# Performance work log

Hardware: AMD Instinct MI355X
Metric: run time of the kernel (lower is better)

## Reference

```python
import jax, jax.numpy as jnp
import numpy as np

D_MODEL = 2048
N_HEAD = 16
SEM_DIM = 1024
GEO_DIM = 1024
ATTN_DIM = 2048
ROPE_BASE = 10000.0


def _rope(x, base=ROPE_BASE):
    # x: [B, H, S, d] with even d; GPT-NeoX rotate-half convention
    S, d = x.shape[-2], x.shape[-1]
    inv_freq = 1.0 / (base ** (jnp.arange(0, d, 2, dtype=jnp.float32) / d))
    t = jnp.arange(S, dtype=jnp.float32)
    freqs = jnp.einsum('s,f->sf', t, inv_freq)  # [S, d/2]
    cos, sin = jnp.cos(freqs), jnp.sin(freqs)
    x1, x2 = x[..., : d // 2], x[..., d // 2 :]
    return jnp.concatenate([x1 * cos - x2 * sin, x1 * sin + x2 * cos], axis=-1).astype(x.dtype)


def _split_heads(y, H):
    B, S, dim = y.shape
    return y.reshape(B, S, H, dim // H).transpose(0, 2, 1, 3)  # [B,H,S,hd]


def setup_inputs() -> dict:
    key = jax.random.key(0)
    ks = jax.random.split(key, 7)
    B, S = 2, 2048
    sd = 0.02
    return {
        'x': jax.random.normal(ks[0], (B, S, D_MODEL), dtype=jnp.float32),
        'Wq_sem': jax.random.normal(ks[1], (SEM_DIM, D_MODEL), dtype=jnp.float32) * sd,
        'Wk_sem': jax.random.normal(ks[2], (SEM_DIM, D_MODEL), dtype=jnp.float32) * sd,
        'Wq_geo': jax.random.normal(ks[3], (GEO_DIM, D_MODEL), dtype=jnp.float32) * sd,
        'Wk_geo': jax.random.normal(ks[4], (GEO_DIM, D_MODEL), dtype=jnp.float32) * sd,
        'Wv': jax.random.normal(ks[5], (ATTN_DIM, D_MODEL), dtype=jnp.float32) * sd,
        'Wo': jax.random.normal(ks[6], (D_MODEL, ATTN_DIM), dtype=jnp.float32) * sd,
    }


def reference(x, Wq_sem, Wk_sem, Wq_geo, Wk_geo, Wv, Wo):
    B, S, _ = x.shape
    H = N_HEAD
    # decoupled projections (nn.Linear: y = x @ W.T)
    q_sem = _split_heads(x @ Wq_sem.T, H)  # [B,H,S,64]
    k_sem = _split_heads(x @ Wk_sem.T, H)
    q_geo = _rope(_split_heads(x @ Wq_geo.T, H))  # RoPE only on geo part
    k_geo = _rope(_split_heads(x @ Wk_geo.T, H))
    v = _split_heads(x @ Wv.T, H)  # [B,H,S,128]
    # concatenated decoupled q/k -> single fused score (fp32), SDPA default scale
    q = jnp.concatenate([q_sem, q_geo], axis=-1)
    k = jnp.concatenate([k_sem, k_geo], axis=-1)
    scale = 1.0 / jnp.sqrt(jnp.asarray(q.shape[-1], dtype=jnp.float32))
    scores = jnp.einsum('bhqd,bhkd->bhqk', q, k).astype(jnp.float32) * scale
    causal = jnp.tril(jnp.ones((S, S), dtype=bool))
    scores = jnp.where(causal, scores, jnp.finfo(jnp.float32).min)
    attn = jax.nn.softmax(scores, axis=-1).astype(v.dtype)
    out = jnp.einsum('bhqk,bhkd->bhqd', attn, v)  # [B,H,S,128]
    out = out.transpose(0, 2, 1, 3).reshape(B, S, ATTN_DIM)
    return out @ Wo.T  # [B,S,d_model]
```

## Files before the change

### kernel.cpp

```cpp
#include <hip/hip_runtime.h>
#include <cstdint>
#include <cstddef>

typedef unsigned short u16;
typedef __attribute__((ext_vector_type(8))) short bf16x8;
typedef __attribute__((ext_vector_type(4))) float f32x4;

#define MFMA32(a, b, c) __builtin_amdgcn_mfma_f32_16x16x32_bf16(a, b, c, 0, 0, 0)

__device__ __forceinline__ u16 f2b(float f) {
  union { float f; unsigned u; } v; v.f = f;
  unsigned u = v.u;
  return (u16)((u + 0x7fffu + ((u >> 16) & 1u)) >> 16);
}
__device__ __forceinline__ float b2f(u16 h) {
  union { unsigned u; float f; } v; v.u = ((unsigned)h) << 16;
  return v.f;
}

__device__ __forceinline__ void g2l16(const void* g, void* l) {
  __builtin_amdgcn_global_load_lds((__attribute__((address_space(1))) void*)(g),
                                   (__attribute__((address_space(3))) void*)(l), 16, 0, 0);
}

__global__ __launch_bounds__(256) void cast_f2b_v4(const float* __restrict__ in,
                                                   u16* __restrict__ out, int n4) {
  int i = blockIdx.x * 256 + threadIdx.x;
  if (i >= n4) return;
  float4 v = ((const float4*)in)[i];
  ushort4 r;
  r.x = f2b(v.x); r.y = f2b(v.y); r.z = f2b(v.z); r.w = f2b(v.w);
  ((ushort4*)out)[i] = r;
}

__global__ __launch_bounds__(256) void cast_weights(const float* __restrict__ W0,
                                                    const float* __restrict__ W1,
                                                    const float* __restrict__ W2,
                                                    const float* __restrict__ W3,
                                                    const float* __restrict__ Wv,
                                                    const float* __restrict__ Wo,
                                                    u16* __restrict__ Wall,
                                                    u16* __restrict__ Wob) {
  const int blk = blockIdx.x;
  const float* src;
  u16* dst;
  int li;
  if (blk < 8192) {
    const int s = blk >> 11;
    src = s == 0 ? W0 : s == 1 ? W1 : s == 2 ? W2 : W3;
    dst = Wall + (size_t)s * 2097152;
    li = (blk & 2047) * 256 + threadIdx.x;
  } else if (blk < 12288) {
    src = Wv;
    dst = Wall + (size_t)4 * 2097152;
    li = (blk - 8192) * 256 + threadIdx.x;
  } else {
    src = Wo;
    dst = Wob;
    li = (blk - 12288) * 256 + threadIdx.x;
  }
  float4 v = ((const float4*)src)[li];
  ushort4 r;
  r.x = f2b(v.x); r.y = f2b(v.y); r.z = f2b(v.z); r.w = f2b(v.w);
  ((ushort4*)dst)[li] = r;
}

template <bool BF16_OUT>
__global__ __launch_bounds__(256) void gemm_bt(const u16* __restrict__ A,
                                               const u16* __restrict__ B,
                                               void* __restrict__ C, int N, int K) {
  __shared__ u16 As[128 * 64];
  __shared__ u16 Bs[128 * 64];
  const int tid = threadIdx.x;
  const int wid = tid >> 6;
  const int lane = tid & 63;
  const int lm = lane & 15;
  const int quad = lane >> 4;
  const int r3 = lm & 7;
  const int wm = (wid & 1) * 64;
  const int wn = (wid >> 1) * 64;
  const int bm = blockIdx.y * 128;
  const int bn = blockIdx.x * 128;

  const u16* Ab = A + (size_t)bm * K;
  const u16* Bb = B + (size_t)bn * K;

  f32x4 zero = {0.f, 0.f, 0.f, 0.f};
  f32x4 acc[4][4];
#pragma unroll
  for (int i = 0; i < 4; ++i)
#pragma unroll
    for (int j = 0; j < 4; ++j) acc[i][j] = zero;

  for (int k0 = 0; k0 < K; k0 += 64) {
#pragma unroll
    for (int it = 0; it < 4; ++it) {
      int c = it * 256 + tid;
      int rg = c >> 6, rw = (c >> 3) & 7, u = c & 7;
      int row = rg * 8 + rw;
      int chd = u ^ rw;
      g2l16(Ab + (size_t)row * K + k0 + chd * 8, As + c * 8);
      g2l16(Bb + (size_t)row * K + k0 + chd * 8, Bs + c * 8);
    }
    __syncthreads();
#pragma unroll
    for (int ks = 0; ks < 2; ++ks) {
      bf16x8 a[4], b[4];
      int chd = ks * 4 + quad;
#pragma unroll
      for (int i = 0; i < 4; ++i) {
        int row = wm + i * 16 + lm;
        a[i] = *(const bf16x8*)(As + (((row >> 3) * 64 + r3 * 8 + (chd ^ r3)) * 8));
      }
#pragma unroll
      for (int j = 0; j < 4; ++j) {
        int row = wn + j * 16 + lm;
        b[j] = *(const bf16x8*)(Bs + (((row >> 3) * 64 + r3 * 8 + (chd ^ r3)) * 8));
      }
#pragma unroll
      for (int i = 0; i < 4; ++i)
#pragma unroll
        for (int j = 0; j < 4; ++j)
          acc[i][j] = MFMA32(a[i], b[j], acc[i][j]);
    }
    __syncthreads();
  }

#pragma unroll
  for (int i = 0; i < 4; ++i)
#pragma unroll
    for (int j = 0; j < 4; ++j)
#pragma unroll
      for (int r = 0; r < 4; ++r) {
        int row = bm + wm + i * 16 + quad * 4 + r;
        int col = bn + wn + j * 16 + lm;
        float v = acc[i][j][r];
        if (BF16_OUT)
          ((u16*)C)[(size_t)row * N + col] = f2b(v);
        else
          ((float*)C)[(size_t)row * N + col] = v;
      }
}

__global__ __launch_bounds__(256) void rope_rearrange_v2(const u16* __restrict__ Y,
                                                         u16* __restrict__ Q,
                                                         u16* __restrict__ Kb,
                                                         u16* __restrict__ VT) {
  const float SC = 0.12751744f;
  __shared__ u16 T[128][68];
  const int st = blockIdx.x;
  const int bh = blockIdx.y;
  const int b = bh >> 4, h = bh & 15;
  const int tid = threadIdx.x;
  const int d = tid & 127;
  const int sgrp = tid >> 7;

  float inv = 0.f;
  const int f0 = d & 31;
  if (d >= 64) inv = __powf(10000.0f, -(float)(2 * f0) * (1.0f / 64.0f));

  const u16* Yc = Y + (size_t)(b * 2048 + st * 64) * 6144;

#pragma unroll 4
  for (int k = 0; k < 32; ++k) {
    const int sl = sgrp * 32 + k;
    const int s = st * 64 + sl;
    const u16* Yr = Yc + (size_t)sl * 6144;

    T[d][sl] = Yr[4096 + h * 128 + d];

    float qv, kv;
    if (d < 64) {
      qv = b2f(Yr[h * 64 + d]);
      kv = b2f(Yr[1024 + h * 64 + d]);
    } else {
      float ang = (float)s * inv;
      float sn = sinf(ang), cs = cosf(ang);
      float qx1 = b2f(Yr[2048 + h * 64 + f0]);
      float qx2 = b2f(Yr[2048 + h * 64 + f0 + 32]);
      float kx1 = b2f(Yr[3072 + h * 64 + f0]);
      float kx2 = b2f(Yr[3072 + h * 64 + f0 + 32]);
      if (d < 96) { qv = qx1 * cs - qx2 * sn; kv = kx1 * cs - kx2 * sn; }
      else        { qv = qx1 * sn + qx2 * cs; kv = kx1 * sn + kx2 * cs; }
    }
    size_t qo = ((size_t)bh * 2048 + s) * 128 + d;
    Q[qo] = f2b(qv * SC);
    Kb[qo] = f2b(kv);
  }
  __syncthreads();

#pragma unroll
  for (int it = 0; it < 8; ++it) {
    const int i = it * 256 + tid;
    const int dd = i >> 4;
    const int ch = i & 15;
    ushort4 v = *(const ushort4*)(&T[dd][ch * 4]);
    *(ushort4*)(VT + ((size_t)bh * 128 + dd) * 2048 + st * 64 + ch * 4) = v;
  }
}

__global__ __launch_bounds__(256, 2) void attn_v8(const u16* __restrict__ Q,
                                                  const u16* __restrict__ K,
                                                  const u16* __restrict__ VT,
                                                  u16* __restrict__ O) {
  constexpr int S = 2048;
  constexpr int D = 128;
  __shared__ u16 Ks[2][64 * 128];
  __shared__ u16 Vs[2][128 * 64];
  __shared__ u16 Ps[64 * 72];
  const int linear = blockIdx.x + (blockIdx.y << 4);
  const int xcd = linear & 7;
  const int slot = linear >> 3;
  const int bh = (xcd << 2) + (slot >> 4);
  const int bx = slot & 15;
  const int b = bh >> 4, h = bh & 15;
  const int tid = threadIdx.x, wid = tid >> 6, lane = tid & 63;
  const int lm = lane & 15, quad = lane >> 4;
  const int rx = lm & 7;
  const int wrow = wid * 16;

  const u16* Kbh = K + (size_t)bh * S * D;
  const u16* Vbh = VT + (size_t)bh * D * S;

  auto stageKV = [&](int kt, int bufid) {
    const u16* Kt = Kbh + (size_t)kt * 64 * D;
    const u16* Vt = Vbh + (size_t)kt * 64;
#pragma unroll
    for (int it = 0; it < 4; ++it) {
      int c = it * 256 + tid;
      int row = c >> 4, u = c & 15;
      g2l16(Kt + (size_t)row * 128 + (size_t)(u ^ (row & 7)) * 8, &Ks[bufid][c * 8]);
    }
#pragma unroll
    for (int it = 0; it < 4; ++it) {
      int c = it * 256 + tid;
      int row = c >> 3, u = c & 7;
      g2l16(Vt + (size_t)row * S + (size_t)(u ^ (row & 7)) * 8, &Vs[bufid][c * 8]);
    }
  };

#pragma unroll 1
  for (int pass = 0; pass < 2; ++pass) {
    const int qt = pass == 0 ? bx : 31 - bx;

    bf16x8 aq[4];
#pragma unroll
    for (int ks = 0; ks < 4; ++ks)
      aq[ks] = *(const bf16x8*)(Q + ((size_t)bh * S + (size_t)qt * 64 + wrow + lm) * D +
                                ks * 32 + quad * 8);

    float l_r[4] = {0.f, 0.f, 0.f, 0.f};
    f32x4 zero = {0.f, 0.f, 0.f, 0.f};
    f32x4 oacc[8];
#pragma unroll
    for (int t = 0; t < 8; ++t) oacc[t] = zero;

    stageKV(0, 0);
    asm volatile("s_waitcnt vmcnt(0)" ::: "memory");
    __builtin_amdgcn_s_barrier();

#pragma unroll 1
    for (int kt = 0; kt <= qt; ++kt) {
      const int cur = kt & 1;
      if (kt < qt) stageKV(kt + 1, cur ^ 1);

      f32x4 sc[4];
#pragma unroll
      for (int j = 0; j < 4; ++j) sc[j] = zero;
      __builtin_amdgcn_s_setprio(1);
#pragma unroll
      for (int ks = 0; ks < 4; ++ks) {
        const int kc = ks * 4 + quad;
#pragma unroll
        for (int j = 0; j < 4; ++j) {
          bf16x8 bk = *(const bf16x8*)(&Ks[cur][((j * 16 + lm) * 16 + (kc ^ rx)) * 8]);
          sc[j] = MFMA32(aq[ks], bk, sc[j]);
        }
      }
      __builtin_amdgcn_s_setprio(0);

      const bool diag = (kt == qt);
#pragma unroll
      for (int r = 0; r < 4; ++r) {
        const int qcol = wrow + quad * 4 + r;
        float pv[4];
        float rs = 0.f;
#pragma unroll
        for (int j = 0; j < 4; ++j) {
          float p = __builtin_amdgcn_exp2f(fminf(sc[j][r], 30.0f));
          if (diag && (j * 16 + lm > qcol)) p = 0.f;
          rs += p;
          pv[j] = p;
        }
#pragma unroll
        for (int dd = 1; dd < 16; dd <<= 1) rs += __shfl_xor(rs, dd);
        l_r[r] += rs;
        const int prow = (wrow + quad * 4 + r) * 72;
#pragma unroll
        for (int j = 0; j < 4; ++j) Ps[prow + j * 16 + lm] = f2b(pv[j]);
      }

      __builtin_amdgcn_s_setprio(1);
#pragma unroll
      for (int ks = 0; ks < 2; ++ks) {
        bf16x8 ap = *(const bf16x8*)(Ps + (wrow + lm) * 72 + ks * 32 + quad * 8);
        const int kc = ks * 4 + quad;
#pragma unroll
        for (int t = 0; t < 8; ++t) {
          bf16x8 bv = *(const bf16x8*)(&Vs[cur][((t * 16 + lm) * 8 + (kc ^ rx)) * 8]);
          oacc[t] = MFMA32(ap, bv, oacc[t]);
        }
      }
      __builtin_amdgcn_s_setprio(0);

      if (kt < qt) asm volatile("s_waitcnt vmcnt(0)" ::: "memory");
      __builtin_amdgcn_s_barrier();
    }

#pragma unroll
    for (int r = 0; r < 4; ++r) {
      float inv = 1.0f / l_r[r];
      const int srow = qt * 64 + wrow + quad * 4 + r;
      u16* Orow = O + ((size_t)b * S + srow) * 2048 + h * 128;
#pragma unroll
      for (int t = 0; t < 8; ++t) Orow[t * 16 + lm] = f2b(oacc[t][r] * inv);
    }
  }
}

extern "C" void kernel_launch(void* const* d_in, const int* in_sizes, int n_in,
                              void* d_out, int out_size, void* d_ws, size_t ws_size,
                              hipStream_t stream) {
  const float* x      = (const float*)d_in[0];
  const float* Wq_sem = (const float*)d_in[1];
  const float* Wk_sem = (const float*)d_in[2];
  const float* Wq_geo = (const float*)d_in[3];
  const float* Wk_geo = (const float*)d_in[4];
  const float* Wv     = (const float*)d_in[5];
  const float* Wo     = (const float*)d_in[6];

  char* ws = (char*)d_ws;
  u16* xb   = (u16*)(ws);
  u16* Wall = (u16*)(ws + 16777216);
  u16* Wob  = (u16*)(ws + 16777216 + 25165824);
  u16* Y    = (u16*)(ws + 16777216 + 25165824 + 8388608);
  u16* Qb   = xb;
  u16* Ob   = Wall;
  u16* Kb   = (u16*)d_out;
  u16* VT   = (u16*)((char*)d_out + 16777216);

  cast_f2b_v4<<<8192, 256, 0, stream>>>(x, xb, 2097152);
  cast_weights<<<16384, 256, 0, stream>>>(Wq_sem, Wk_sem, Wq_geo, Wk_geo, Wv, Wo, Wall, Wob);

  gemm_bt<true><<<dim3(48, 32), 256, 0, stream>>>(xb, Wall, Y, 6144, 2048);

  rope_rearrange_v2<<<dim3(32, 32), 256, 0, stream>>>(Y, Qb, Kb, VT);

  attn_v8<<<dim3(16, 32), 256, 0, stream>>>(Qb, Kb, VT, Ob);

  gemm_bt<false><<<dim3(16, 32), 256, 0, stream>>>(Ob, Wob, d_out, 2048, 2048);
}
```

Baseline: 391.8 us.

## Use 256x256-tile eight-wave pipelined GEMM for fused QKV projection

Adds a new bf16 GEMM kernel with 256x256 block tiles, 512 threads and 128KB of double-buffered dynamic LDS. It uses XOR-swizzled direct global-to-LDS loads, staged in quarter-tile chunks interleaved with the MFMA sub-phases. Barriers, explicit vmcnt waits and raised wave priority overlap memory traffic with compute. The aim is more data reuse per LDS byte and fewer global reloads for the large projection GEMM. The cost is a 384-block grid on 256 CUs, which leaves an uneven tail, plus heavy register and LDS pressure that limits occupancy.

```diff
diff --git a/kernel.cpp b/kernel.cpp
--- a/kernel.cpp
+++ b/kernel.cpp
@@ -142,6 +142,152 @@
       }
 }
 
+__global__ __launch_bounds__(512, 2) void gemm_bt8(const u16* __restrict__ A,
+                                                   const u16* __restrict__ B,
+                                                   u16* __restrict__ C, int N, int K) {
+  extern __shared__ char smem[];
+  u16* sA = (u16*)smem;
+  u16* sB = (u16*)(smem + 65536);
+  const int tid = threadIdx.x;
+  const int wid = tid >> 6, lane = tid & 63;
+  const int lm = lane & 15, quad = lane >> 4, rx = lm & 7;
+  const int wm = wid >> 2;
+  const int wn = wid & 3;
+  const int bm = blockIdx.y * 256, bn = blockIdx.x * 256;
+  const u16* Ablk = A + (size_t)bm * K;
+  const u16* Bblk = B + (size_t)bn * K;
+
+  f32x4 zero = {0.f, 0.f, 0.f, 0.f};
+  f32x4 acc[8][4];
+#pragma unroll
+  for (int i = 0; i < 8; ++i)
+#pragma unroll
+    for (int j = 0; j < 4; ++j) acc[i][j] = zero;
+
+  bf16x8 aA[4][2];
+  bf16x8 bB[2][2][2];
+
+  const int NT = K >> 6;
+  const int NH = NT << 2;
+  const int NIT = NT >> 1;
+
+  auto stageh = [&](int q) {
+    const int st = q >> 2, sh = q & 3;
+    const int k0 = st << 6;
+    const int bf = st & 1;
+    const u16* src;
+    u16* dst;
+    int rowbase;
+    if (sh < 2) { src = Ablk; rowbase = sh << 7; dst = sA + (bf * 2 + sh) * 8192; }
+    else        { src = Bblk; rowbase = (sh - 2) << 7; dst = sB + (bf * 2 + (sh - 2)) * 8192; }
+#pragma unroll
+    for (int it = 0; it < 2; ++it) {
+      const int c = it * 512 + tid;
+      const int r = c >> 3, u = c & 7;
+      g2l16(src + (size_t)(rowbase + r) * K + k0 + ((u ^ (r & 7)) << 3), dst + (size_t)c * 8);
+    }
+  };
+  auto ldA = [&](int bf, int mh) {
+    const u16* Ah = sA + (bf * 2 + wm) * 8192;
+#pragma unroll
+    for (int ii = 0; ii < 4; ++ii)
+#pragma unroll
+      for (int ks = 0; ks < 2; ++ks)
+        aA[ii][ks] = *(const bf16x8*)(Ah + ((((mh * 4 + ii) * 16 + lm) * 8 +
+                                             ((ks * 4 + quad) ^ rx)) << 3));
+  };
+  auto ldB = [&](int bf, int nh) {
+    const u16* Bh = sB + (bf * 2 + (wn >> 1)) * 8192;
+#pragma unroll
+    for (int jj = 0; jj < 2; ++jj)
+#pragma unroll
+      for (int ks = 0; ks < 2; ++ks)
+        bB[nh][jj][ks] = *(const bf16x8*)(Bh + ((((wn & 1) * 64 + (nh * 2 + jj) * 16 + lm) * 8 +
+                                                 ((ks * 4 + quad) ^ rx)) << 3));
+  };
+  auto mm = [&](int mh, int nh) {
+    __builtin_amdgcn_s_setprio(1);
+#pragma unroll
+    for (int ii = 0; ii < 4; ++ii)
+#pragma unroll
+      for (int jj = 0; jj < 2; ++jj)
+#pragma unroll
+        for (int ks = 0; ks < 2; ++ks)
+          acc[mh * 4 + ii][nh * 2 + jj] =
+              MFMA32(aA[ii][ks], bB[nh][jj][ks], acc[mh * 4 + ii][nh * 2 + jj]);
+    __builtin_amdgcn_s_setprio(0);
+  };
+
+#pragma unroll
+  for (int q = 0; q < 5; ++q) stageh(q);
+  asm volatile("s_waitcnt vmcnt(2)" ::: "memory");
+  __builtin_amdgcn_s_barrier();
+
+#pragma unroll 1
+  for (int i = 0; i < NIT; ++i) {
+    const int qb = 8 * i;
+    ldA(0, 0); ldB(0, 0);
+    if (qb + 5 < NH) stageh(qb + 5);
+    __builtin_amdgcn_s_barrier();
+    mm(0, 0);
+    __builtin_amdgcn_s_barrier();
+    ldB(0, 1);
+    if (qb + 6 < NH) stageh(qb + 6);
+    __builtin_amdgcn_s_barrier();
+    mm(0, 1);
+    __builtin_amdgcn_s_barrier();
+    ldA(0, 1);
+    if (qb + 7 < NH) stageh(qb + 7);
+    __builtin_amdgcn_s_barrier();
+    mm(1, 1);
+    __builtin_amdgcn_s_barrier();
+    {
+      const bool st = (qb + 8 < NH);
+      if (st) stageh(qb + 8);
+      __builtin_amdgcn_s_barrier();
+      mm(1, 0);
+      if (st) asm volatile("s_waitcnt vmcnt(2)" ::: "memory");
+      else    asm volatile("s_waitcnt vmcnt(0)" ::: "memory");
+      __builtin_amdgcn_s_barrier();
+    }
+    ldA(1, 0); ldB(1, 0);
+    if (qb + 9 < NH) stageh(qb + 9);
+    __builtin_amdgcn_s_barrier();
+    mm(0, 0);
+    __builtin_amdgcn_s_barrier();
+    ldB(1, 1);
+    if (qb + 10 < NH) stageh(qb + 10);
+    __builtin_amdgcn_s_barrier();
+    mm(0, 1);
+    __builtin_amdgcn_s_barrier();
+    ldA(1, 1);
+    if (qb + 11 < NH) stageh(qb + 11);
+    __builtin_amdgcn_s_barrier();
+    mm(1, 1);
+    __builtin_amdgcn_s_barrier();
+    {
+      const bool st = (qb + 12 < NH);
+      if (st) stageh(qb + 12);
+      __builtin_amdgcn_s_barrier();
+      mm(1, 0);
+      if (st) asm volatile("s_waitcnt vmcnt(2)" ::: "memory");
+      else    asm volatile("s_waitcnt vmcnt(0)" ::: "memory");
+      __builtin_amdgcn_s_barrier();
+    }
+  }
+
+#pragma unroll
+  for (int ii = 0; ii < 8; ++ii)
+#pragma unroll
+    for (int jj = 0; jj < 4; ++jj)
+#pragma unroll
+      for (int r = 0; r < 4; ++r) {
+        const int row = bm + wm * 128 + ii * 16 + quad * 4 + r;
+        const int col = bn + wn * 64 + jj * 16 + lm;
+        C[(size_t)row * N + col] = f2b(acc[ii][jj][r]);
+      }
+}
+
 __global__ __launch_bounds__(256) void rope_rearrange_v2(const u16* __restrict__ Y,
                                                          u16* __restrict__ Q,
                                                          u16* __restrict__ Kb,
@@ -349,10 +495,13 @@
   u16* Kb   = (u16*)d_out;
   u16* VT   = (u16*)((char*)d_out + 16777216);
 
+  hipFuncSetAttribute((const void*)gemm_bt8,
+                      hipFuncAttributeMaxDynamicSharedMemorySize, 131072);
+
   cast_f2b_v4<<<8192, 256, 0, stream>>>(x, xb, 2097152);
   cast_weights<<<16384, 256, 0, stream>>>(Wq_sem, Wk_sem, Wq_geo, Wk_geo, Wv, Wo, Wall, Wob);
 
-  gemm_bt<true><<<dim3(48, 32), 256, 0, stream>>>(xb, Wall, Y, 6144, 2048);
+  gemm_bt8<<<dim3(24, 16), 512, 131072, stream>>>(xb, Wall, Y, 6144, 2048);
 
   rope_rearrange_v2<<<dim3(32, 32), 256, 0, stream>>>(Y, Qb, Kb, VT);
 
```

New measurement: 391.7 us. Within noise of the previous version (-0.0%).

## Fuse RoPE, head split and V transpose into QKV projection GEMM epilogue

Applied to the files above, without the earlier changes.

Replaces the separate QKV GEMM plus rope_rearrange kernel with a single GEMM whose epilogue writes Q/K directly in head-major layout, applies RoPE with sincos in registers, and transposes V through shared memory into VT. This removes the round trip of the 6144-wide Y intermediate through global memory and one kernel launch. In exchange, the epilogue writes are scattered 2-byte stores and the V path adds extra syncs, and Q moves to a separate workspace buffer.

```diff
diff --git a/kernel.cpp b/kernel.cpp
--- a/kernel.cpp
+++ b/kernel.cpp
@@ -142,60 +142,144 @@
       }
 }
 
-__global__ __launch_bounds__(256) void rope_rearrange_v2(const u16* __restrict__ Y,
-                                                         u16* __restrict__ Q,
-                                                         u16* __restrict__ Kb,
-                                                         u16* __restrict__ VT) {
+__global__ __launch_bounds__(256) void gemm_qkv(const u16* __restrict__ A,
+                                                const u16* __restrict__ B,
+                                                u16* __restrict__ Qb,
+                                                u16* __restrict__ Kb,
+                                                u16* __restrict__ VT) {
+  constexpr int K = 2048;
   const float SC = 0.12751744f;
-  __shared__ u16 T[128][68];
-  const int st = blockIdx.x;
-  const int bh = blockIdx.y;
-  const int b = bh >> 4, h = bh & 15;
+  __shared__ u16 sh[16384];
+  u16* As = sh;
+  u16* Bs = sh + 8192;
   const int tid = threadIdx.x;
-  const int d = tid & 127;
-  const int sgrp = tid >> 7;
-
-  float inv = 0.f;
-  const int f0 = d & 31;
-  if (d >= 64) inv = __powf(10000.0f, -(float)(2 * f0) * (1.0f / 64.0f));
-
-  const u16* Yc = Y + (size_t)(b * 2048 + st * 64) * 6144;
-
-#pragma unroll 4
-  for (int k = 0; k < 32; ++k) {
-    const int sl = sgrp * 32 + k;
-    const int s = st * 64 + sl;
-    const u16* Yr = Yc + (size_t)sl * 6144;
-
-    T[d][sl] = Yr[4096 + h * 128 + d];
-
-    float qv, kv;
-    if (d < 64) {
-      qv = b2f(Yr[h * 64 + d]);
-      kv = b2f(Yr[1024 + h * 64 + d]);
-    } else {
-      float ang = (float)s * inv;
-      float sn = sinf(ang), cs = cosf(ang);
-      float qx1 = b2f(Yr[2048 + h * 64 + f0]);
-      float qx2 = b2f(Yr[2048 + h * 64 + f0 + 32]);
-      float kx1 = b2f(Yr[3072 + h * 64 + f0]);
-      float kx2 = b2f(Yr[3072 + h * 64 + f0 + 32]);
-      if (d < 96) { qv = qx1 * cs - qx2 * sn; kv = kx1 * cs - kx2 * sn; }
-      else        { qv = qx1 * sn + qx2 * cs; kv = kx1 * sn + kx2 * cs; }
-    }
-    size_t qo = ((size_t)bh * 2048 + s) * 128 + d;
-    Q[qo] = f2b(qv * SC);
-    Kb[qo] = f2b(kv);
+  const int wid = tid >> 6;
+  const int lane = tid & 63;
+  const int lm = lane & 15;
+  const int quad = lane >> 4;
+  const int r3 = lm & 7;
+  const int wm = (wid & 1) * 64;
+  const int wn = (wid >> 1) * 64;
+  const int bm = blockIdx.y * 128;
+  const int bn = blockIdx.x * 128;
+
+  const u16* Ab = A + (size_t)bm * K;
+  const u16* Bb = B + (size_t)bn * K;
+
+  f32x4 zero = {0.f, 0.f, 0.f, 0.f};
+  f32x4 acc[4][4];
+#pragma unroll
+  for (int i = 0; i < 4; ++i)
+#pragma unroll
+    for (int j = 0; j < 4; ++j) acc[i][j] = zero;
+
+  for (int k0 = 0; k0 < K; k0 += 64) {
+#pragma unroll
+    for (int it = 0; it < 4; ++it) {
+      int c = it * 256 + tid;
+      int rg = c >> 6, rw = (c >> 3) & 7, u = c & 7;
+      int row = rg * 8 + rw;
+      int chd = u ^ rw;
+      g2l16(Ab + (size_t)row * K + k0 + chd * 8, As + c * 8);
+      g2l16(Bb + (size_t)row * K + k0 + chd * 8, Bs + c * 8);
+    }
+    __syncthreads();
+#pragma unroll
+    for (int ks = 0; ks < 2; ++ks) {
+      bf16x8 a[4], b[4];
+      int chd = ks * 4 + quad;
+#pragma unroll
+      for (int i = 0; i < 4; ++i) {
+        int row = wm + i * 16 + lm;
+        a[i] = *(const bf16x8*)(As + (((row >> 3) * 64 + r3 * 8 + (chd ^ r3)) * 8));
+      }
+#pragma unroll
+      for (int j = 0; j < 4; ++j) {
+        int row = wn + j * 16 + lm;
+        b[j] = *(const bf16x8*)(Bs + (((row >> 3) * 64 + r3 * 8 + (chd ^ r3)) * 8));
+      }
+#pragma unroll
+      for (int i = 0; i < 4; ++i)
+#pragma unroll
+        for (int j = 0; j < 4; ++j)
+          acc[i][j] = MFMA32(a[i], b[j], acc[i][j]);
+    }
+    __syncthreads();
   }
-  __syncthreads();
-
-#pragma unroll
-  for (int it = 0; it < 8; ++it) {
-    const int i = it * 256 + tid;
-    const int dd = i >> 4;
-    const int ch = i & 15;
-    ushort4 v = *(const ushort4*)(&T[dd][ch * 4]);
-    *(ushort4*)(VT + ((size_t)bh * 128 + dd) * 2048 + st * 64 + ch * 4) = v;
+
+  const int seg = bn >> 10;
+  const int b = bm >> 11;
+  const int sbase = bm & 2047;
+  const int h = ((bn + wn) >> 6) & 15;
+  const size_t bhQ = (size_t)b * 16 + h;
+
+  if (seg < 2) {
+    u16* dst = (seg == 0) ? Qb : Kb;
+    const float sc = (seg == 0) ? SC : 1.0f;
+#pragma unroll
+    for (int i = 0; i < 4; ++i)
+#pragma unroll
+      for (int r = 0; r < 4; ++r) {
+        const int s = sbase + wm + i * 16 + quad * 4 + r;
+        u16* base = dst + (bhQ * 2048 + s) * 128;
+#pragma unroll
+        for (int j = 0; j < 4; ++j) {
+          const int d = (wn + j * 16 + lm) & 63;
+          base[d] = f2b(acc[i][j][r] * sc);
+        }
+      }
+  } else if (seg < 4) {
+    u16* dst = (seg == 2) ? Qb : Kb;
+    const float sc = (seg == 2) ? SC : 1.0f;
+    const float inv0 = __powf(10000.0f, -(float)(2 * lm) * (1.0f / 64.0f));
+    const float inv1 = __powf(10000.0f, -(float)(2 * (16 + lm)) * (1.0f / 64.0f));
+#pragma unroll
+    for (int i = 0; i < 4; ++i)
+#pragma unroll
+      for (int r = 0; r < 4; ++r) {
+        const int s = sbase + wm + i * 16 + quad * 4 + r;
+        float sn0, cs0, sn1, cs1;
+        __sincosf((float)s * inv0, &sn0, &cs0);
+        __sincosf((float)s * inv1, &sn1, &cs1);
+        const float x1a = acc[i][0][r], x2a = acc[i][2][r];
+        const float x1b = acc[i][1][r], x2b = acc[i][3][r];
+        u16* base = dst + (bhQ * 2048 + s) * 128 + 64;
+        base[lm]      = f2b((x1a * cs0 - x2a * sn0) * sc);
+        base[16 + lm] = f2b((x1b * cs1 - x2b * sn1) * sc);
+        base[32 + lm] = f2b((x1a * sn0 + x2a * cs0) * sc);
+        base[48 + lm] = f2b((x1b * sn1 + x2b * cs1) * sc);
+      }
+  } else {
+    const int hv = (bn - 4096) >> 7;
+    const size_t bh = (size_t)b * 16 + hv;
+    u16(*buf)[66] = (u16(*)[66])sh;
+    const int myhalf = wn >> 6;
+#pragma unroll 1
+    for (int half = 0; half < 2; ++half) {
+      __syncthreads();
+      if (myhalf == half) {
+#pragma unroll
+        for (int i = 0; i < 4; ++i)
+#pragma unroll
+          for (int j = 0; j < 4; ++j)
+#pragma unroll
+            for (int r = 0; r < 4; ++r)
+              buf[wm + i * 16 + quad * 4 + r][j * 16 + lm] = f2b(acc[i][j][r]);
+      }
+      __syncthreads();
+#pragma unroll
+      for (int it = 0; it < 8; ++it) {
+        const int idx = it * 256 + tid;
+        const int dd = idx >> 5;
+        const int sc4 = idx & 31;
+        ushort4 v;
+        v.x = buf[sc4 * 4 + 0][dd];
+        v.y = buf[sc4 * 4 + 1][dd];
+        v.z = buf[sc4 * 4 + 2][dd];
+        v.w = buf[sc4 * 4 + 3][dd];
+        *(ushort4*)(VT + (bh * 128 + half * 64 + dd) * 2048 + sbase + sc4 * 4) = v;
+      }
+    }
   }
 }
 
@@ -343,8 +427,7 @@
   u16* xb   = (u16*)(ws);
   u16* Wall = (u16*)(ws + 16777216);
   u16* Wob  = (u16*)(ws + 16777216 + 25165824);
-  u16* Y    = (u16*)(ws + 16777216 + 25165824 + 8388608);
-  u16* Qb   = xb;
+  u16* Qb   = (u16*)(ws + 16777216 + 25165824 + 8388608);
   u16* Ob   = Wall;
   u16* Kb   = (u16*)d_out;
   u16* VT   = (u16*)((char*)d_out + 16777216);
@@ -352,9 +435,7 @@
   cast_f2b_v4<<<8192, 256, 0, stream>>>(x, xb, 2097152);
   cast_weights<<<16384, 256, 0, stream>>>(Wq_sem, Wk_sem, Wq_geo, Wk_geo, Wv, Wo, Wall, Wob);
 
-  gemm_bt<true><<<dim3(48, 32), 256, 0, stream>>>(xb, Wall, Y, 6144, 2048);
-
-  rope_rearrange_v2<<<dim3(32, 32), 256, 0, stream>>>(Y, Qb, Kb, VT);
+  gemm_qkv<<<dim3(48, 32), 256, 0, stream>>>(xb, Wall, Qb, Kb, VT);
 
   attn_v8<<<dim3(16, 32), 256, 0, stream>>>(Qb, Kb, VT, Ob);
 
```

After: 373.2 us. 1.05x faster.
